# Performance work log

Hardware: AMD Instinct MI355X
Metric: run time of the kernel (lower is better)

The kernel has to match this reference:

```python
import jax, jax.numpy as jnp
import numpy as np

# Profile-HMM forward-backward in log space.
# inputs : (M, B, L, S) soft/one-hot observation features
# log_A  : (M, Q, Q) row-stochastic log transition matrix
# log_pi : (M, Q)    log initial distribution
# log_B  : (M, Q, S) log emission matrix

M, B, L, Q, S = 1, 64, 2048, 256, 26
EPS = 1e-16


def setup_inputs() -> dict:
    key = jax.random.key(0)
    k1, k2, k3, k4 = jax.random.split(key, 4)
    inputs = jax.random.uniform(k1, (M, B, L, S), dtype=jnp.float32)
    log_A = jax.nn.log_softmax(jax.random.normal(k2, (M, Q, Q), dtype=jnp.float32), axis=-1)
    log_pi = jax.nn.log_softmax(jax.random.normal(k3, (M, Q), dtype=jnp.float32), axis=-1)
    log_B = jax.nn.log_softmax(jax.random.normal(k4, (M, Q, S), dtype=jnp.float32), axis=-1)
    return {"inputs": inputs, "log_A": log_A, "log_pi": log_pi, "log_B": log_B}


def _forward_backward(inputs, log_A, log_pi, log_B):
    # emission probs per state: e[m,b,l,q] = sum_s inputs[m,b,l,s] * B[m,q,s]
    emit = jnp.einsum('mbls,mqs->mblq', inputs, jnp.exp(log_B))
    log_e = jnp.log(emit + EPS)
    log_e_t = jnp.moveaxis(log_e, 2, 0)  # (L, M, B, Q) time-major

    # forward recursion: alpha_t[i] = logsumexp_j(alpha_{t-1}[j] + A[j,i]) + e_t[i]
    alpha0 = log_pi[:, None, :] + log_e_t[0]  # (M, B, Q)

    def fstep(alpha, le):
        new = jax.nn.logsumexp(alpha[..., :, None] + log_A[:, None], axis=-2) + le
        return new, new

    _, alphas = jax.lax.scan(fstep, alpha0, log_e_t[1:])
    alphas = jnp.concatenate([alpha0[None], alphas], axis=0)  # (L, M, B, Q)

    # backward recursion: beta_t[i] = logsumexp_j(A[i,j] + e_{t+1}[j] + beta_{t+1}[j])
    beta_last = jnp.zeros_like(alpha0)

    def bstep(beta, le):
        new = jax.nn.logsumexp(log_A[:, None] + (le + beta)[:, :, None, :], axis=-1)
        return new, new

    _, betas = jax.lax.scan(bstep, beta_last, log_e_t[1:], reverse=True)
    betas = jnp.concatenate([betas, beta_last[None]], axis=0)  # (L, M, B, Q)

    loglik = jax.nn.logsumexp(alphas[-1], axis=-1)  # (M, B)
    post = alphas + betas - loglik[None, :, :, None]  # state posterior log probs
    return jnp.moveaxis(post, 0, 2), loglik  # (M, B, L, Q), (M, B)


def reference(inputs, log_A, log_pi, log_B):
    post, loglik = _forward_backward(inputs, log_A, log_pi, log_B)
    return post, loglik
```

## Files before the change

kernel.cpp:

```cpp
#include <hip/hip_runtime.h>

namespace {

constexpr int B = 64;
constexpr int L = 2048;
constexpr int Q = 256;
constexpr int S = 26;
constexpr float EPS = 1e-16f;
constexpr size_t POST = (size_t)B * L * Q;

typedef _Float16 h2 __attribute__((ext_vector_type(2)));
typedef _Float16 f16x8 __attribute__((ext_vector_type(8)));
typedef float f32x4 __attribute__((ext_vector_type(4)));

#define MFMA16(a, b, c) __builtin_amdgcn_mfma_f32_16x16x32_f16((a), (b), (c), 0, 0, 0)

struct Smem {
  alignas(16) _Float16 vb[2][Q];
  alignas(16) _Float16 rowh[2][32];
  alignas(16) _Float16 rowl[2][32];
  float sh[2];
  alignas(16) float afin[Q];
};

__device__ __forceinline__ float wave_max64(float x) {
#pragma unroll
  for (int off = 32; off > 0; off >>= 1) x = fmaxf(x, __shfl_xor(x, off, 64));
  return x;
}
__device__ __forceinline__ float wave_sum64(float x) {
#pragma unroll
  for (int off = 32; off > 0; off >>= 1) x += __shfl_xor(x, off, 64);
  return x;
}

__device__ __forceinline__ void load_emit_frags(const float* __restrict__ log_B,
                                                int c0, int c1, int g, int q,
                                                f16x8& Bh0, f16x8& Bl0,
                                                f16x8& Bh1, f16x8& Bl1) {
#pragma unroll
  for (int j = 0; j < 8; ++j) {
    const int s = g * 8 + j;
    const float v0 = (s < S) ? __expf(log_B[(size_t)(c0 + q) * S + s]) : 0.f;
    const float v1 = (s < S) ? __expf(log_B[(size_t)(c1 + q) * S + s]) : 0.f;
    const _Float16 h0 = (_Float16)v0, h1 = (_Float16)v1;
    Bh0[j] = h0; Bl0[j] = (_Float16)(v0 - (float)h0);
    Bh1[j] = h1; Bl1[j] = (_Float16)(v1 - (float)h1);
  }
}

__device__ __forceinline__ void stage_row(Smem& sm, int buf, int lane, float2 gg) {
  _Float16 ah = (_Float16)0.f, bh = (_Float16)0.f;
  _Float16 al = (_Float16)0.f, bl = (_Float16)0.f;
  if (lane < 13) {
    ah = (_Float16)gg.x; bh = (_Float16)gg.y;
    al = (_Float16)(gg.x - (float)ah);
    bl = (_Float16)(gg.y - (float)bh);
  }
  ((h2*)sm.rowh[buf])[lane] = h2{ah, bh};
  ((h2*)sm.rowl[buf])[lane] = h2{al, bl};
}

__device__ __forceinline__ void emit_mfma(const f16x8& xh, const f16x8& xl,
                                          const f16x8& Bh0, const f16x8& Bl0,
                                          const f16x8& Bh1, const f16x8& Bl1,
                                          f32x4& E0, f32x4& E1) {
  const f32x4 Z = {0.f, 0.f, 0.f, 0.f};
  E0 = MFMA16(xh, Bl0, Z);
  E0 = MFMA16(xl, Bh0, E0);
  E0 = MFMA16(xh, Bh0, E0);
  E1 = MFMA16(xh, Bl1, Z);
  E1 = MFMA16(xl, Bh1, E1);
  E1 = MFMA16(xh, Bh1, E1);
}

__device__ __forceinline__ void matvec_mfma(const f16x8* va, const f16x8* T0,
                                            const f16x8* T1, float& x0, float& x1) {
  const f32x4 Z = {0.f, 0.f, 0.f, 0.f};
  f32x4 X0a = MFMA16(va[0], T0[0], Z);
  f32x4 X1a = MFMA16(va[0], T1[0], Z);
  f32x4 X0b = MFMA16(va[4], T0[4], Z);
  f32x4 X1b = MFMA16(va[4], T1[4], Z);
#pragma unroll
  for (int f = 1; f < 4; ++f) {
    X0a = MFMA16(va[f], T0[f], X0a);
    X1a = MFMA16(va[f], T1[f], X1a);
    X0b = MFMA16(va[f + 4], T0[f + 4], X0b);
    X1b = MFMA16(va[f + 4], T1[f + 4], X1b);
  }
  x0 = X0a[0] + X0b[0];
  x1 = X1a[0] + X1b[0];
}

__device__ __forceinline__ void read_frags(Smem& sm, int p, int g,
                                           f16x8& xh, f16x8& xl, f16x8* va) {
  xh = *(const f16x8*)(sm.rowh[p] + g * 8);
  xl = *(const f16x8*)(sm.rowl[p] + g * 8);
  const _Float16* vbp = sm.vb[p];
#pragma unroll
  for (int f = 0; f < 8; ++f) va[f] = *(const f16x8*)(vbp + f * 32 + g * 8);
}

__device__ __forceinline__ void fwd_impl(int b, const float* __restrict__ inputs,
                                         const float* __restrict__ log_A,
                                         const float* __restrict__ log_pi,
                                         const float* __restrict__ log_B,
                                         float* __restrict__ out, Smem& sm) {
  const int tid = threadIdx.x, w = tid >> 6, lane = tid & 63;
  const int g = lane >> 4, q = lane & 15;
  const int c0 = w * 32, c1 = c0 + 16;
  const bool rdl = (q == 0);
  const bool epi = (lane < 16);
  const bool stg = (w == 0) && (lane < 16);

  f16x8 T0[8], T1[8];
#pragma unroll
  for (int f = 0; f < 8; ++f) {
#pragma unroll
    for (int j = 0; j < 8; ++j) {
      const int k = f * 32 + g * 8 + j;
      T0[f][j] = (_Float16)__expf(log_A[(size_t)k * Q + c0 + q]);
      T1[f][j] = (_Float16)__expf(log_A[(size_t)k * Q + c1 + q]);
    }
  }
  f16x8 Bh0, Bl0, Bh1, Bl1;
  load_emit_frags(log_B, c0, c1, g, q, Bh0, Bl0, Bh1, Bl1);

  const float2* __restrict__ inp2 = (const float2*)(inputs + (size_t)b * L * S);
  float* __restrict__ post_b = out + (size_t)b * L * Q;

  if (stg) {
    float2 g0, g1;
    if (lane < 13) { g0 = inp2[lane]; g1 = inp2[13 + lane]; }
    stage_row(sm, 1, lane, g0);
    stage_row(sm, 0, lane, g1);
  }
  __syncthreads();

  f16x8 xh = {}, xl = {};
  f16x8 va[8];
#pragma unroll
  for (int f = 0; f < 8; ++f) va[f] = f16x8{};

  if (rdl) {
    xh = *(const f16x8*)(sm.rowh[1] + g * 8);
    xl = *(const f16x8*)(sm.rowl[1] + g * 8);
  }
  f32x4 E0, E1;
  emit_mfma(xh, xl, Bh0, Bl0, Bh1, Bl1, E0, E1);
  float zh0 = 1.f, zh1 = 1.f, rdp_h = 0.f;
  if (epi) {
    zh0 = (E0[0] + EPS) * __expf(log_pi[c0 + lane]);
    zh1 = (E1[0] + EPS) * __expf(log_pi[c1 + lane]);
  }
  if (tid == 0) sm.sh[0] = __logf(zh0);
  __syncthreads();
  float rd_prev = sm.sh[0];
  if (epi) {
    const float sc = __expf(-rd_prev);
    sm.vb[0][c0 + lane] = (_Float16)(zh0 * sc);
    sm.vb[0][c1 + lane] = (_Float16)(zh1 * sc);
  }
  __syncthreads();

  int p = 0;
  for (int t = 1; t < L; ++t) {
    const float rd = sm.sh[p];
    float2 gg;
    const int tt = (t + 1 < L) ? t + 1 : L - 1;
    if (w == 0 && lane < 13) gg = inp2[(size_t)tt * 13 + lane];
    if (epi) {
      const float a0 = __logf(zh0) + rdp_h;
      const float a1 = __logf(zh1) + rdp_h;
      post_b[(size_t)(t - 1) * Q + c0 + lane] = a0;
      post_b[(size_t)(t - 1) * Q + c1 + lane] = a1;
    }
    if (rdl) read_frags(sm, p, g, xh, xl, va);
    f32x4 E0_, E1_;
    emit_mfma(xh, xl, Bh0, Bl0, Bh1, Bl1, E0_, E1_);
    float x0, x1;
    matvec_mfma(va, T0, T1, x0, x1);
    const float gam = __expf(rd_prev - rd);
    if (epi) {
      const float e0 = E0_[0] + EPS, e1 = E1_[0] + EPS;
      const float z0 = x0 * e0, z1 = x1 * e1;
      sm.vb[p ^ 1][c0 + lane] = (_Float16)(z0 * gam);
      sm.vb[p ^ 1][c1 + lane] = (_Float16)(z1 * gam);
      if (tid == 0) sm.sh[p ^ 1] = __logf(z0) + rd_prev;
      zh0 = z0; zh1 = z1;
    }
    rdp_h = rd_prev;
    rd_prev = rd;
    if (stg) stage_row(sm, p ^ 1, lane, gg);
    __syncthreads();
    p ^= 1;
  }

  if (epi) {
    const float a0 = __logf(zh0) + rdp_h;
    const float a1 = __logf(zh1) + rdp_h;
    post_b[(size_t)(L - 1) * Q + c0 + lane] = a0;
    post_b[(size_t)(L - 1) * Q + c1 + lane] = a1;
    sm.afin[c0 + lane] = a0;
    sm.afin[c1 + lane] = a1;
  }
  __syncthreads();
  if (w == 0) {
    float4 fa = ((const float4*)sm.afin)[lane];
    float m = fmaxf(fmaxf(fa.x, fa.y), fmaxf(fa.z, fa.w));
    m = wave_max64(m);
    float ss = __expf(fa.x - m) + __expf(fa.y - m) + __expf(fa.z - m) + __expf(fa.w - m);
    ss = wave_sum64(ss);
    if (lane == 0) out[POST + b] = __logf(ss) + m;
  }
}

template <int MODE>
__device__ __forceinline__ void bwd_impl(int b, const float* __restrict__ inputs,
                                         const float* __restrict__ log_A,
                                         const float* __restrict__ log_B,
                                         float* __restrict__ out,
                                         float* __restrict__ ws, Smem& sm) {
  const int tid = threadIdx.x, w = tid >> 6, lane = tid & 63;
  const int g = lane >> 4, q = lane & 15;
  const int c0 = w * 32, c1 = c0 + 16;
  const bool rdl = (q == 0);
  const bool epi = (lane < 16);
  const bool stg = (w == 0) && (lane < 16);

  f16x8 T0[8], T1[8];
#pragma unroll
  for (int f = 0; f < 8; ++f) {
#pragma unroll
    for (int j = 0; j < 8; ++j) {
      const int k = f * 32 + g * 8 + j;
      T0[f][j] = (_Float16)__expf(log_A[(size_t)(c0 + q) * Q + k]);
      T1[f][j] = (_Float16)__expf(log_A[(size_t)(c1 + q) * Q + k]);
    }
  }
  f16x8 Bh0, Bl0, Bh1, Bl1;
  load_emit_frags(log_B, c0, c1, g, q, Bh0, Bl0, Bh1, Bl1);

  const float2* __restrict__ inp2 = (const float2*)(inputs + (size_t)b * L * S);
  float* __restrict__ post_b = out + (size_t)b * L * Q;
  float* __restrict__ ws_b = ws + (size_t)b * L * Q;

  float ll = 0.f, a_h0 = 0.f, a_h1 = 0.f;
  if (MODE == 1) {
    ll = out[POST + b];
    if (epi) {
      a_h0 = post_b[(size_t)(L - 1) * Q + c0 + lane];
      a_h1 = post_b[(size_t)(L - 1) * Q + c1 + lane];
    }
  }

  if (stg) {
    float2 g0, g1;
    if (lane < 13) {
      g0 = inp2[(size_t)(L - 1) * 13 + lane];
      g1 = inp2[(size_t)(L - 2) * 13 + lane];
    }
    stage_row(sm, 1, lane, g0);
    stage_row(sm, 0, lane, g1);
  }
  __syncthreads();

  f16x8 xh = {}, xl = {};
  f16x8 va[8];
#pragma unroll
  for (int f = 0; f < 8; ++f) va[f] = f16x8{};

  if (rdl) {
    xh = *(const f16x8*)(sm.rowh[1] + g * 8);
    xl = *(const f16x8*)(sm.rowl[1] + g * 8);
  }
  f32x4 E0, E1;
  emit_mfma(xh, xl, Bh0, Bl0, Bh1, Bl1, E0, E1);
  float e0i = 1.f, e1i = 1.f;
  if (epi) { e0i = E0[0] + EPS; e1i = E1[0] + EPS; }
  if (tid == 0) sm.sh[0] = __logf(e0i);
  __syncthreads();
  float rd_prev = sm.sh[0];
  if (epi) {
    const float sc = __expf(-rd_prev);
    sm.vb[0][c0 + lane] = (_Float16)(e0i * sc);
    sm.vb[0][c1 + lane] = (_Float16)(e1i * sc);
  }
  float rh0 = 1.f, rh1 = 1.f, rdp_h = 0.f;
  __syncthreads();

  int p = 0;
  for (int t = L - 2; t >= 0; --t) {
    const float rd = sm.sh[p];
    float2 gg;
    const int tt = (t > 0) ? t - 1 : 0;
    if (w == 0 && lane < 13) gg = inp2[(size_t)tt * 13 + lane];
    if (epi) {
      const float b0 = __logf(rh0) + rdp_h;
      const float b1 = __logf(rh1) + rdp_h;
      if (MODE == 0) {
        ws_b[(size_t)(t + 1) * Q + c0 + lane] = b0;
        ws_b[(size_t)(t + 1) * Q + c1 + lane] = b1;
      } else {
        post_b[(size_t)(t + 1) * Q + c0 + lane] = a_h0 + b0 - ll;
        post_b[(size_t)(t + 1) * Q + c1 + lane] = a_h1 + b1 - ll;
        a_h0 = post_b[(size_t)t * Q + c0 + lane];
        a_h1 = post_b[(size_t)t * Q + c1 + lane];
      }
    }
    if (rdl) read_frags(sm, p, g, xh, xl, va);
    f32x4 E0_, E1_;
    emit_mfma(xh, xl, Bh0, Bl0, Bh1, Bl1, E0_, E1_);
    float r0, r1;
    matvec_mfma(va, T0, T1, r0, r1);
    const float gam = __expf(rd_prev - rd);
    if (epi) {
      const float e0 = E0_[0] + EPS, e1 = E1_[0] + EPS;
      const float z0 = r0 * e0, z1 = r1 * e1;
      sm.vb[p ^ 1][c0 + lane] = (_Float16)(z0 * gam);
      sm.vb[p ^ 1][c1 + lane] = (_Float16)(z1 * gam);
      if (tid == 0) sm.sh[p ^ 1] = __logf(z0) + rd_prev;
      rh0 = r0; rh1 = r1;
    }
    rdp_h = rd_prev;
    rd_prev = rd;
    if (stg) stage_row(sm, p ^ 1, lane, gg);
    __syncthreads();
    p ^= 1;
  }

  if (epi) {
    const float b0 = __logf(rh0) + rdp_h;
    const float b1 = __logf(rh1) + rdp_h;
    if (MODE == 0) {
      ws_b[c0 + lane] = b0;
      ws_b[c1 + lane] = b1;
    } else {
      post_b[c0 + lane] = a_h0 + b0 - ll;
      post_b[c1 + lane] = a_h1 + b1 - ll;
    }
  }
}

__global__ __launch_bounds__(512, 2)
void hmm_fwdbwd(const float* __restrict__ inputs, const float* __restrict__ log_A,
                const float* __restrict__ log_pi, const float* __restrict__ log_B,
                float* __restrict__ out, float* __restrict__ ws) {
  __shared__ Smem sm;
  if (blockIdx.x < B) fwd_impl(blockIdx.x, inputs, log_A, log_pi, log_B, out, sm);
  else                bwd_impl<0>(blockIdx.x - B, inputs, log_A, log_B, out, ws, sm);
}

__global__ __launch_bounds__(256)
void hmm_combine(const float* __restrict__ ws, float* __restrict__ out) {
  const size_t idx = (size_t)blockIdx.x * 256 + threadIdx.x;
  const int b = (int)(idx >> 17);
  const float ll = out[POST + b];
  float4 a = ((const float4*)out)[idx];
  const float4 be = ((const float4*)ws)[idx];
  a.x += be.x - ll;
  a.y += be.y - ll;
  a.z += be.z - ll;
  a.w += be.w - ll;
  ((float4*)out)[idx] = a;
}

__global__ __launch_bounds__(512, 2)
void hmm_fwd_only(const float* __restrict__ inputs, const float* __restrict__ log_A,
                  const float* __restrict__ log_pi, const float* __restrict__ log_B,
                  float* __restrict__ out) {
  __shared__ Smem sm;
  fwd_impl(blockIdx.x, inputs, log_A, log_pi, log_B, out, sm);
}

__global__ __launch_bounds__(512, 2)
void hmm_bwd_fused(const float* __restrict__ inputs, const float* __restrict__ log_A,
                   const float* __restrict__ log_B, float* __restrict__ out) {
  __shared__ Smem sm;
  bwd_impl<1>(blockIdx.x, inputs, log_A, log_B, out, nullptr, sm);
}

}

extern "C" void kernel_launch(void* const* d_in, const int* in_sizes, int n_in,
                              void* d_out, int out_size, void* d_ws, size_t ws_size,
                              hipStream_t stream) {
  const float* inputs = (const float*)d_in[0];
  const float* log_A  = (const float*)d_in[1];
  const float* log_pi = (const float*)d_in[2];
  const float* log_B  = (const float*)d_in[3];
  float* out = (float*)d_out;
  float* ws  = (float*)d_ws;

  if (ws_size >= POST * sizeof(float)) {
    hipLaunchKernelGGL(hmm_fwdbwd, dim3(2 * B), dim3(512), 0, stream,
                       inputs, log_A, log_pi, log_B, out, ws);
    hipLaunchKernelGGL(hmm_combine, dim3((unsigned)(POST / 4 / 256)), dim3(256), 0, stream,
                       ws, out);
  } else {
    hipLaunchKernelGGL(hmm_fwd_only, dim3(B), dim3(512), 0, stream,
                       inputs, log_A, log_pi, log_B, out);
    hipLaunchKernelGGL(hmm_bwd_fused, dim3(B), dim3(512), 0, stream,
                       inputs, log_A, log_B, out);
  }
}
```

Baseline: 1.630 ms.

## Prefetch observation rows into registers and use LDS-only barriers

Each fragment-reading lane now loads its own slice of the next observation row from global memory one step ahead and splits it into fp16 hi/lo halves in registers. This replaces the path where wave 0 staged the converted row through shared memory. Every __syncthreads in the forward and backward recursions becomes a barrier that waits only on LDS counters (lgkmcnt), not on outstanding global loads and stores. The goal is to keep global stores of posteriors and the input prefetch off the per-step critical path. In exchange, more lanes issue global loads and the code relies on the compiler inserting vmcnt waits before the prefetched values are used.

Result: slower. 1.743 ms (+7.0%).

```diff
diff --git a/kernel.cpp b/kernel.cpp
--- a/kernel.cpp
+++ b/kernel.cpp
@@ -9,7 +9,6 @@
 constexpr float EPS = 1e-16f;
 constexpr size_t POST = (size_t)B * L * Q;
 
-typedef _Float16 h2 __attribute__((ext_vector_type(2)));
 typedef _Float16 f16x8 __attribute__((ext_vector_type(8)));
 typedef float f32x4 __attribute__((ext_vector_type(4)));
 
@@ -17,11 +16,13 @@
 
 struct Smem {
   alignas(16) _Float16 vb[2][Q];
-  alignas(16) _Float16 rowh[2][32];
-  alignas(16) _Float16 rowl[2][32];
   float sh[2];
   alignas(16) float afin[Q];
 };
+
+__device__ __forceinline__ void lds_barrier() {
+  asm volatile("s_waitcnt lgkmcnt(0)\n\ts_barrier" ::: "memory");
+}
 
 __device__ __forceinline__ float wave_max64(float x) {
 #pragma unroll
@@ -49,16 +50,23 @@
   }
 }
 
-__device__ __forceinline__ void stage_row(Smem& sm, int buf, int lane, float2 gg) {
-  _Float16 ah = (_Float16)0.f, bh = (_Float16)0.f;
-  _Float16 al = (_Float16)0.f, bl = (_Float16)0.f;
-  if (lane < 13) {
-    ah = (_Float16)gg.x; bh = (_Float16)gg.y;
-    al = (_Float16)(gg.x - (float)ah);
-    bl = (_Float16)(gg.y - (float)bh);
-  }
-  ((h2*)sm.rowh[buf])[lane] = h2{ah, bh};
-  ((h2*)sm.rowl[buf])[lane] = h2{al, bl};
+__device__ __forceinline__ void load_row(const float* __restrict__ row, int g,
+                                         bool rdl, float2* ld) {
+  if (rdl) {
+    const float2* r2 = (const float2*)(row + g * 8);
+    ld[0] = r2[0];
+    if (g < 3) { ld[1] = r2[1]; ld[2] = r2[2]; ld[3] = r2[3]; }
+  }
+}
+
+__device__ __forceinline__ void cvt_row(const float2* ld, f16x8& xh, f16x8& xl) {
+#pragma unroll
+  for (int i = 0; i < 4; ++i) {
+    const float a = ld[i].x, bb = ld[i].y;
+    const _Float16 ah = (_Float16)a, bh = (_Float16)bb;
+    xh[2 * i] = ah;     xl[2 * i] = (_Float16)(a - (float)ah);
+    xh[2 * i + 1] = bh; xl[2 * i + 1] = (_Float16)(bb - (float)bh);
+  }
 }
 
 __device__ __forceinline__ void emit_mfma(const f16x8& xh, const f16x8& xl,
@@ -92,10 +100,7 @@
   x1 = X1a[0] + X1b[0];
 }
 
-__device__ __forceinline__ void read_frags(Smem& sm, int p, int g,
-                                           f16x8& xh, f16x8& xl, f16x8* va) {
-  xh = *(const f16x8*)(sm.rowh[p] + g * 8);
-  xl = *(const f16x8*)(sm.rowl[p] + g * 8);
+__device__ __forceinline__ void read_frags(Smem& sm, int p, int g, f16x8* va) {
   const _Float16* vbp = sm.vb[p];
 #pragma unroll
   for (int f = 0; f < 8; ++f) va[f] = *(const f16x8*)(vbp + f * 32 + g * 8);
@@ -111,7 +116,6 @@
   const int c0 = w * 32, c1 = c0 + 16;
   const bool rdl = (q == 0);
   const bool epi = (lane < 16);
-  const bool stg = (w == 0) && (lane < 16);
 
   f16x8 T0[8], T1[8];
 #pragma unroll
@@ -126,56 +130,48 @@
   f16x8 Bh0, Bl0, Bh1, Bl1;
   load_emit_frags(log_B, c0, c1, g, q, Bh0, Bl0, Bh1, Bl1);
 
-  const float2* __restrict__ inp2 = (const float2*)(inputs + (size_t)b * L * S);
+  const float* __restrict__ rowbase = inputs + (size_t)b * L * S;
   float* __restrict__ post_b = out + (size_t)b * L * Q;
 
-  if (stg) {
-    float2 g0, g1;
-    if (lane < 13) { g0 = inp2[lane]; g1 = inp2[13 + lane]; }
-    stage_row(sm, 1, lane, g0);
-    stage_row(sm, 0, lane, g1);
-  }
-  __syncthreads();
-
+  float2 ld[4] = {{0.f, 0.f}, {0.f, 0.f}, {0.f, 0.f}, {0.f, 0.f}};
   f16x8 xh = {}, xl = {};
   f16x8 va[8];
 #pragma unroll
   for (int f = 0; f < 8; ++f) va[f] = f16x8{};
 
-  if (rdl) {
-    xh = *(const f16x8*)(sm.rowh[1] + g * 8);
-    xl = *(const f16x8*)(sm.rowl[1] + g * 8);
-  }
+  load_row(rowbase, g, rdl, ld);
+  cvt_row(ld, xh, xl);
   f32x4 E0, E1;
   emit_mfma(xh, xl, Bh0, Bl0, Bh1, Bl1, E0, E1);
+  load_row(rowbase + S, g, rdl, ld);
   float zh0 = 1.f, zh1 = 1.f, rdp_h = 0.f;
   if (epi) {
     zh0 = (E0[0] + EPS) * __expf(log_pi[c0 + lane]);
     zh1 = (E1[0] + EPS) * __expf(log_pi[c1 + lane]);
   }
   if (tid == 0) sm.sh[0] = __logf(zh0);
-  __syncthreads();
+  lds_barrier();
   float rd_prev = sm.sh[0];
   if (epi) {
     const float sc = __expf(-rd_prev);
     sm.vb[0][c0 + lane] = (_Float16)(zh0 * sc);
     sm.vb[0][c1 + lane] = (_Float16)(zh1 * sc);
   }
-  __syncthreads();
+  lds_barrier();
 
   int p = 0;
   for (int t = 1; t < L; ++t) {
     const float rd = sm.sh[p];
-    float2 gg;
+    if (rdl) read_frags(sm, p, g, va);
+    cvt_row(ld, xh, xl);
     const int tt = (t + 1 < L) ? t + 1 : L - 1;
-    if (w == 0 && lane < 13) gg = inp2[(size_t)tt * 13 + lane];
+    load_row(rowbase + (size_t)tt * S, g, rdl, ld);
     if (epi) {
       const float a0 = __logf(zh0) + rdp_h;
       const float a1 = __logf(zh1) + rdp_h;
       post_b[(size_t)(t - 1) * Q + c0 + lane] = a0;
       post_b[(size_t)(t - 1) * Q + c1 + lane] = a1;
     }
-    if (rdl) read_frags(sm, p, g, xh, xl, va);
     f32x4 E0_, E1_;
     emit_mfma(xh, xl, Bh0, Bl0, Bh1, Bl1, E0_, E1_);
     float x0, x1;
@@ -191,8 +187,7 @@
     }
     rdp_h = rd_prev;
     rd_prev = rd;
-    if (stg) stage_row(sm, p ^ 1, lane, gg);
-    __syncthreads();
+    lds_barrier();
     p ^= 1;
   }
 
@@ -204,7 +199,7 @@
     sm.afin[c0 + lane] = a0;
     sm.afin[c1 + lane] = a1;
   }
-  __syncthreads();
+  lds_barrier();
   if (w == 0) {
     float4 fa = ((const float4*)sm.afin)[lane];
     float m = fmaxf(fmaxf(fa.x, fa.y), fmaxf(fa.z, fa.w));
@@ -226,7 +221,6 @@
   const int c0 = w * 32, c1 = c0 + 16;
   const bool rdl = (q == 0);
   const bool epi = (lane < 16);
-  const bool stg = (w == 0) && (lane < 16);
 
   f16x8 T0[8], T1[8];
 #pragma unroll
@@ -241,7 +235,7 @@
   f16x8 Bh0, Bl0, Bh1, Bl1;
   load_emit_frags(log_B, c0, c1, g, q, Bh0, Bl0, Bh1, Bl1);
 
-  const float2* __restrict__ inp2 = (const float2*)(inputs + (size_t)b * L * S);
+  const float* __restrict__ rowbase = inputs + (size_t)b * L * S;
   float* __restrict__ post_b = out + (size_t)b * L * Q;
   float* __restrict__ ws_b = ws + (size_t)b * L * Q;
 
@@ -254,32 +248,21 @@
     }
   }
 
-  if (stg) {
-    float2 g0, g1;
-    if (lane < 13) {
-      g0 = inp2[(size_t)(L - 1) * 13 + lane];
-      g1 = inp2[(size_t)(L - 2) * 13 + lane];
-    }
-    stage_row(sm, 1, lane, g0);
-    stage_row(sm, 0, lane, g1);
-  }
-  __syncthreads();
-
+  float2 ld[4] = {{0.f, 0.f}, {0.f, 0.f}, {0.f, 0.f}, {0.f, 0.f}};
   f16x8 xh = {}, xl = {};
   f16x8 va[8];
 #pragma unroll
   for (int f = 0; f < 8; ++f) va[f] = f16x8{};
 
-  if (rdl) {
-    xh = *(const f16x8*)(sm.rowh[1] + g * 8);
-    xl = *(const f16x8*)(sm.rowl[1] + g * 8);
-  }
+  load_row(rowbase + (size_t)(L - 1) * S, g, rdl, ld);
+  cvt_row(ld, xh, xl);
   f32x4 E0, E1;
   emit_mfma(xh, xl, Bh0, Bl0, Bh1, Bl1, E0, E1);
+  load_row(rowbase + (size_t)(L - 2) * S, g, rdl, ld);
   float e0i = 1.f, e1i = 1.f;
   if (epi) { e0i = E0[0] + EPS; e1i = E1[0] + EPS; }
   if (tid == 0) sm.sh[0] = __logf(e0i);
-  __syncthreads();
+  lds_barrier();
   float rd_prev = sm.sh[0];
   if (epi) {
     const float sc = __expf(-rd_prev);
@@ -287,14 +270,15 @@
     sm.vb[0][c1 + lane] = (_Float16)(e1i * sc);
   }
   float rh0 = 1.f, rh1 = 1.f, rdp_h = 0.f;
-  __syncthreads();
+  lds_barrier();
 
   int p = 0;
   for (int t = L - 2; t >= 0; --t) {
     const float rd = sm.sh[p];
-    float2 gg;
+    if (rdl) read_frags(sm, p, g, va);
+    cvt_row(ld, xh, xl);
     const int tt = (t > 0) ? t - 1 : 0;
-    if (w == 0 && lane < 13) gg = inp2[(size_t)tt * 13 + lane];
+    load_row(rowbase + (size_t)tt * S, g, rdl, ld);
     if (epi) {
       const float b0 = __logf(rh0) + rdp_h;
       const float b1 = __logf(rh1) + rdp_h;
@@ -308,7 +292,6 @@
         a_h1 = post_b[(size_t)t * Q + c1 + lane];
       }
     }
-    if (rdl) read_frags(sm, p, g, xh, xl, va);
     f32x4 E0_, E1_;
     emit_mfma(xh, xl, Bh0, Bl0, Bh1, Bl1, E0_, E1_);
     float r0, r1;
@@ -324,8 +307,7 @@
     }
     rdp_h = rd_prev;
     rd_prev = rd;
-    if (stg) stage_row(sm, p ^ 1, lane, gg);
-    __syncthreads();
+    lds_barrier();
     p ^= 1;
   }
 
```
